# Optimization experiments

Measured on AMD Instinct MI355X. Metric: run time of the kernel, lower is better.

The kernel has to match this reference:

```python
import jax, jax.numpy as jnp
import numpy as np

N_NODES = 100000
N_EDGES = 640000
IN_DIM = 64
HIDDEN = 128
N_STEPS = 5
NUM_CLASSES = 2


def _gru_cell(a, h, w_ih, w_hh, b_ih, b_hh):
    # PyTorch GRUCell: gates ordered (reset, update, new)
    gi = a @ w_ih.T + b_ih   # [N, 3H]
    gh = h @ w_hh.T + b_hh   # [N, 3H]
    i_r, i_z, i_n = jnp.split(gi, 3, axis=-1)
    h_r, h_z, h_n = jnp.split(gh, 3, axis=-1)
    r = jax.nn.sigmoid(i_r + h_r)
    z = jax.nn.sigmoid(i_z + h_z)
    n = jnp.tanh(i_n + r * h_n)
    return (1.0 - z) * n + z * h


def _gated_graph_conv(feat, src, dst, W, b, w_ih, w_hh, b_ih, b_hh):
    # DGL GatedGraphConv with a single edge type:
    #   pad input to out_feats, then n_steps of
    #   a = sum_{incoming edges} Linear(h[src]); h = GRUCell(a, h)
    n = feat.shape[0]
    pad = HIDDEN - feat.shape[1]
    h = jnp.pad(feat, ((0, 0), (0, pad))) if pad > 0 else feat
    for _ in range(N_STEPS):
        m = h @ W.T + b                                  # [N, H] edge-type linear
        a = jax.ops.segment_sum(m[src], dst, num_segments=n)  # gather + scatter-sum
        h = _gru_cell(a, h, w_ih, w_hh, b_ih, b_hh)
    return h


def setup_inputs() -> dict:
    key = jax.random.key(0)
    ks = jax.random.split(key, 16)
    s = 0.05
    inp = {
        "features": jax.random.normal(ks[0], (N_NODES, IN_DIM), dtype=jnp.float32),
        "src": jax.random.randint(ks[1], (N_EDGES,), 0, N_NODES, dtype=jnp.int32),
        "dst": jax.random.randint(ks[2], (N_EDGES,), 0, N_NODES, dtype=jnp.int32),
        # layer 1 (in 64 -> padded to 128)
        "W1": jax.random.normal(ks[3], (HIDDEN, HIDDEN), dtype=jnp.float32) * s,
        "b1": jnp.zeros((HIDDEN,), dtype=jnp.float32),
        "gru1_w_ih": jax.random.normal(ks[4], (3 * HIDDEN, HIDDEN), dtype=jnp.float32) * s,
        "gru1_w_hh": jax.random.normal(ks[5], (3 * HIDDEN, HIDDEN), dtype=jnp.float32) * s,
        "gru1_b_ih": jnp.zeros((3 * HIDDEN,), dtype=jnp.float32),
        "gru1_b_hh": jnp.zeros((3 * HIDDEN,), dtype=jnp.float32),
        # layer 2 (128 -> 128)
        "W2": jax.random.normal(ks[6], (HIDDEN, HIDDEN), dtype=jnp.float32) * s,
        "b2": jnp.zeros((HIDDEN,), dtype=jnp.float32),
        "gru2_w_ih": jax.random.normal(ks[7], (3 * HIDDEN, HIDDEN), dtype=jnp.float32) * s,
        "gru2_w_hh": jax.random.normal(ks[8], (3 * HIDDEN, HIDDEN), dtype=jnp.float32) * s,
        "gru2_b_ih": jnp.zeros((3 * HIDDEN,), dtype=jnp.float32),
        "gru2_b_hh": jnp.zeros((3 * HIDDEN,), dtype=jnp.float32),
        # classifier head
        "fc_w": jax.random.normal(ks[9], (NUM_CLASSES, HIDDEN), dtype=jnp.float32) * s,
        "fc_b": jnp.zeros((NUM_CLASSES,), dtype=jnp.float32),
    }
    return inp


def reference(features, src, dst,
              W1, b1, gru1_w_ih, gru1_w_hh, gru1_b_ih, gru1_b_hh,
              W2, b2, gru2_w_ih, gru2_w_hh, gru2_b_ih, gru2_b_hh,
              fc_w, fc_b):
    h = _gated_graph_conv(features, src, dst, W1, b1, gru1_w_ih, gru1_w_hh, gru1_b_ih, gru1_b_hh)
    h = _gated_graph_conv(h, src, dst, W2, b2, gru2_w_ih, gru2_w_hh, gru2_b_ih, gru2_b_hh)
    return h @ fc_w.T + fc_b  # [N, num_classes]
```

## Files before the change

### kernel.cpp

```cpp
#include <hip/hip_runtime.h>

#define N_HID 128
typedef unsigned short u16;
typedef unsigned int u32;
typedef __attribute__((ext_vector_type(8))) short bfrag;
typedef __attribute__((ext_vector_type(4))) float facc;

__device__ __forceinline__ float sigf(float x) { return 1.f / (1.f + __expf(-x)); }
__device__ __forceinline__ float tanh_fast(float x) { return 1.f - 2.f / (__expf(2.f * x) + 1.f); }
__device__ __forceinline__ u16 f2bf(float f) {
  u32 u = __float_as_uint(f);
  u += 0x7fffu + ((u >> 16) & 1u);
  return (u16)(u >> 16);
}
__device__ __forceinline__ float bf2f(u16 b) { return __uint_as_float(((u32)b) << 16); }

__global__ __launch_bounds__(256) void wihw_kernel(const float* __restrict__ wih,
                                                   const float* __restrict__ W,
                                                   float* __restrict__ out) {
  int i = blockIdx.x * 256 + threadIdx.x;
  if (i >= 49152) return;
  int gc = i >> 7, k = i & 127;
  float acc = 0.f;
  for (int c = 0; c < 128; c++) acc = fmaf(wih[gc * 128 + c], W[c * 128 + k], acc);
  out[i] = acc;
}

__global__ __launch_bounds__(256) void wb_kernel(const float* __restrict__ wih,
                                                 const float* __restrict__ b,
                                                 float* __restrict__ wb) {
  int gc = blockIdx.x * 256 + threadIdx.x;
  if (gc >= 384) return;
  float acc = 0.f;
  for (int c = 0; c < 128; c++) acc = fmaf(wih[gc * 128 + c], b[c], acc);
  wb[gc] = acc;
}

__global__ __launch_bounds__(128) void pack_bias_kernel(const float* __restrict__ bih,
                                                        const float* __restrict__ bhh,
                                                        const float* __restrict__ wb,
                                                        float* __restrict__ PB7) {
  int ch = threadIdx.x;
  PB7[ch * 8 + 0] = bih[ch] + bhh[ch];
  PB7[ch * 8 + 1] = bih[128 + ch] + bhh[128 + ch];
  PB7[ch * 8 + 2] = bih[256 + ch];
  PB7[ch * 8 + 3] = bhh[256 + ch];
  PB7[ch * 8 + 4] = wb[ch];
  PB7[ch * 8 + 5] = wb[128 + ch];
  PB7[ch * 8 + 6] = wb[256 + ch];
  PB7[ch * 8 + 7] = 0.f;
}

__global__ __launch_bounds__(256) void pack_gru_kernel(const float* __restrict__ wih,
                                                       const float* __restrict__ whh,
                                                       u16* __restrict__ GB) {
  int i = blockIdx.x * 256 + threadIdx.x;
  if (i >= 131072) return;
  int e = i & 7, l = (i >> 3) & 63, pct = (i >> 9) & 31, kt = i >> 14;
  int cw = pct >> 3, t = pct & 7, kind = t >> 1, sub = t & 1;
  int ch = cw * 32 + ((l & 15) << 1) + sub;
  int k = kt * 32 + ((l >> 4) << 3) + e;
  float v = 0.f;
  if (kind == 0) v = (k < 128) ? wih[ch * 128 + k] : whh[ch * 128 + k - 128];
  else if (kind == 1) v = (k < 128) ? wih[(128 + ch) * 128 + k] : whh[(128 + ch) * 128 + k - 128];
  else if (kind == 2) v = (k < 128) ? wih[(256 + ch) * 128 + k] : 0.f;
  else v = (k >= 128) ? whh[(256 + ch) * 128 + k - 128] : 0.f;
  GB[i] = f2bf(v);
}

__global__ __launch_bounds__(256) void pad_bf_kernel(const float* __restrict__ feat,
                                                     u16* __restrict__ hbf, int n) {
  int i = blockIdx.x * 256 + threadIdx.x;
  if (i >= n * 32) return;
  int node = i >> 5, c4 = i & 31;
  float4 v = make_float4(0.f, 0.f, 0.f, 0.f);
  if (c4 < 16) v = ((const float4*)feat)[(size_t)node * 16 + c4];
  u32 p0 = (u32)f2bf(v.x) | ((u32)f2bf(v.y) << 16);
  u32 p1 = (u32)f2bf(v.z) | ((u32)f2bf(v.w) << 16);
  ((uint2*)hbf)[i] = make_uint2(p0, p1);
}

__global__ __launch_bounds__(256) void hist_kernel(const int* __restrict__ dst,
                                                   int* __restrict__ deg, int E) {
  int e = blockIdx.x * 256 + threadIdx.x;
  if (e < E) atomicAdd(&deg[dst[e]], 1);
}

__global__ __launch_bounds__(256) void scan1_kernel(const int* __restrict__ deg,
                                                    int* __restrict__ out,
                                                    int* __restrict__ bsums, int n) {
  __shared__ int s[256];
  int t = threadIdx.x;
  int base = blockIdx.x * 4096 + t * 16;
  int v[16];
  int local = 0;
#pragma unroll
  for (int i = 0; i < 16; i++) {
    int x = (base + i < n) ? deg[base + i] : 0;
    v[i] = local;
    local += x;
  }
  s[t] = local;
  __syncthreads();
  for (int off = 1; off < 256; off <<= 1) {
    int add = (t >= off) ? s[t - off] : 0;
    __syncthreads();
    s[t] += add;
    __syncthreads();
  }
  int texcl = s[t] - local;
#pragma unroll
  for (int i = 0; i < 16; i++)
    if (base + i < n) out[base + i] = texcl + v[i];
  if (t == 255) bsums[blockIdx.x] = s[255];
}

__global__ __launch_bounds__(256) void scan_tops_kernel(int* __restrict__ bsums, int nb) {
  __shared__ int s[256];
  int t = threadIdx.x;
  int orig = (t < nb) ? bsums[t] : 0;
  s[t] = orig;
  __syncthreads();
  for (int off = 1; off < 256; off <<= 1) {
    int add = (t >= off) ? s[t - off] : 0;
    __syncthreads();
    s[t] += add;
    __syncthreads();
  }
  if (t < nb) bsums[t] = s[t] - orig;
}

__global__ __launch_bounds__(256) void scan_add_kernel(int* __restrict__ rowptr,
                                                       const int* __restrict__ bsums,
                                                       int n, int E) {
  int i = blockIdx.x * 256 + threadIdx.x;
  if (i < n) rowptr[i] += bsums[i / 4096];
  if (i == n) rowptr[n] = E;
}

__global__ __launch_bounds__(256) void bucket_kernel(const int* __restrict__ src,
                                                     const int* __restrict__ dst,
                                                     const int* __restrict__ rowptr,
                                                     int* __restrict__ cursor,
                                                     int* __restrict__ csr_src, int E) {
  int e = blockIdx.x * 256 + threadIdx.x;
  if (e >= E) return;
  int d = dst[e];
  int p = atomicAdd(&cursor[d], 1);
  csr_src[rowptr[d] + p] = src[e] * 16;
}

__global__ __launch_bounds__(512) void gru_fused_kernel(const u16* __restrict__ hbf_in,
                                                        u16* __restrict__ hbf_out,
                                                        const u16* __restrict__ GB,
                                                        const float* __restrict__ PB7,
                                                        const int* __restrict__ rowptr,
                                                        const int* __restrict__ csr_src,
                                                        const int* __restrict__ deg, int n) {
  __shared__ __align__(16) u16 sX[64 * 256];
  __shared__ float sD[64];
  const int tid = threadIdx.x;
  const int base = blockIdx.x * 64;

  if (tid < 64) {
    int gn = base + tid;
    if (gn >= n) gn = n - 1;
    sD[tid] = (float)deg[gn];
  }
  for (int it = 0; it < 2; it++) {
    int cid = it * 512 + tid;
    int node = cid >> 4, cc = cid & 15;
    int gn = base + node;
    if (gn >= n) gn = n - 1;
    uint4 v = ((const uint4*)hbf_in)[(size_t)gn * 16 + cc];
    int c = 16 + cc;
    *(uint4*)((char*)sX + node * 512 + ((c ^ (node & 7)) << 4)) = v;
  }

  {
    int node = tid >> 3, p = tid & 7;
    int gn = base + node;
    if (gn >= n) gn = n - 1;
    int beg = rowptr[gn], end = rowptr[gn + 1];
    float acc[16];
#pragma unroll
    for (int i = 0; i < 16; i++) acc[i] = 0.f;
#define ACC8(v, o)                                                       \
    acc[o + 0] += bf2f((u16)((v).x & 0xffff)); acc[o + 1] += bf2f((u16)((v).x >> 16)); \
    acc[o + 2] += bf2f((u16)((v).y & 0xffff)); acc[o + 3] += bf2f((u16)((v).y >> 16)); \
    acc[o + 4] += bf2f((u16)((v).z & 0xffff)); acc[o + 5] += bf2f((u16)((v).z >> 16)); \
    acc[o + 6] += bf2f((u16)((v).w & 0xffff)); acc[o + 7] += bf2f((u16)((v).w >> 16));
    const uint4* hp = (const uint4*)hbf_in + 2 * p;
    int j = beg;
    int nA = (j < end) ? csr_src[j] : 0;
    int nB = (j + 1 < end) ? csr_src[j + 1] : 0;
    for (; j + 1 < end; j += 2) {
      int o0 = nA, o1 = nB;
      nA = (j + 2 < end) ? csr_src[j + 2] : 0;
      nB = (j + 3 < end) ? csr_src[j + 3] : 0;
      uint4 a0 = hp[o0];
      uint4 a1 = hp[o0 + 1];
      uint4 b0 = hp[o1];
      uint4 b1 = hp[o1 + 1];
      ACC8(a0, 0); ACC8(a1, 8); ACC8(b0, 0); ACC8(b1, 8);
    }
    if (j < end) {
      int o0 = nA;
      uint4 a0 = hp[o0];
      uint4 a1 = hp[o0 + 1];
      ACC8(a0, 0); ACC8(a1, 8);
    }
#undef ACC8
    uint4 w0, w1;
    w0.x = (u32)f2bf(acc[0])  | ((u32)f2bf(acc[1])  << 16);
    w0.y = (u32)f2bf(acc[2])  | ((u32)f2bf(acc[3])  << 16);
    w0.z = (u32)f2bf(acc[4])  | ((u32)f2bf(acc[5])  << 16);
    w0.w = (u32)f2bf(acc[6])  | ((u32)f2bf(acc[7])  << 16);
    w1.x = (u32)f2bf(acc[8])  | ((u32)f2bf(acc[9])  << 16);
    w1.y = (u32)f2bf(acc[10]) | ((u32)f2bf(acc[11]) << 16);
    w1.z = (u32)f2bf(acc[12]) | ((u32)f2bf(acc[13]) << 16);
    w1.w = (u32)f2bf(acc[14]) | ((u32)f2bf(acc[15]) << 16);
    *(uint4*)((char*)sX + node * 512 + (((2 * p)     ^ (node & 7)) << 4)) = w0;
    *(uint4*)((char*)sX + node * 512 + (((2 * p + 1) ^ (node & 7)) << 4)) = w1;
  }
  __syncthreads();

  const int w = tid >> 6, l = tid & 63;
  const int cw = w & 3, nh = w >> 2;
  facc accR[2][2], accZ[2][2], accIN[2][2], accHN[2][2];
#pragma unroll
  for (int i = 0; i < 2; i++)
#pragma unroll
    for (int j = 0; j < 2; j++) {
      accR[i][j] = (facc)(0.f); accZ[i][j] = (facc)(0.f);
      accIN[i][j] = (facc)(0.f); accHN[i][j] = (facc)(0.f);
    }

#pragma unroll
  for (int kt = 0; kt < 8; kt++) {
    bfrag A[2];
#pragma unroll
    for (int rt = 0; rt < 2; rt++) {
      int row = nh * 32 + rt * 16 + (l & 15);
      int slot = kt * 4 + (l >> 4);
      A[rt] = *(const bfrag*)((const char*)sX + row * 512 + ((slot ^ (row & 7)) << 4));
    }
    const bfrag* gb = (const bfrag*)GB + (size_t)(kt * 32 + cw * 8) * 64 + l;
#pragma unroll
    for (int s2 = 0; s2 < 2; s2++) {
      bfrag Br = gb[s2 * 64];
      bfrag Bz = gb[(2 + s2) * 64];
#pragma unroll
      for (int rt = 0; rt < 2; rt++) {
        accR[rt][s2] = __builtin_amdgcn_mfma_f32_16x16x32_bf16(A[rt], Br, accR[rt][s2], 0, 0, 0);
        accZ[rt][s2] = __builtin_amdgcn_mfma_f32_16x16x32_bf16(A[rt], Bz, accZ[rt][s2], 0, 0, 0);
      }
    }
    if (kt < 4) {
#pragma unroll
      for (int s2 = 0; s2 < 2; s2++) {
        bfrag Bi = gb[(4 + s2) * 64];
#pragma unroll
        for (int rt = 0; rt < 2; rt++)
          accIN[rt][s2] = __builtin_amdgcn_mfma_f32_16x16x32_bf16(A[rt], Bi, accIN[rt][s2], 0, 0, 0);
      }
    } else {
#pragma unroll
      for (int s2 = 0; s2 < 2; s2++) {
        bfrag Bh = gb[(6 + s2) * 64];
#pragma unroll
        for (int rt = 0; rt < 2; rt++)
          accHN[rt][s2] = __builtin_amdgcn_mfma_f32_16x16x32_bf16(A[rt], Bh, accHN[rt][s2], 0, 0, 0);
      }
    }
  }

  {
    int m = l & 15;
    int ch0 = cw * 32 + (m << 1);
    const float4* pb = (const float4*)(PB7 + ch0 * 8);
    float4 c0a = pb[0], c0b = pb[1];
    float4 c1a = pb[2], c1b = pb[3];
    int hc = 16 + (ch0 >> 3);
    int hb = (ch0 & 7) * 2;
#pragma unroll
    for (int rt = 0; rt < 2; rt++)
#pragma unroll
      for (int j = 0; j < 4; j++) {
        int gl = nh * 32 + rt * 16 + ((l >> 4) << 2) + j;
        int g = base + gl;
        float dg = sD[gl];
        u32 hop = *(const u32*)((const char*)sX + gl * 512 + ((hc ^ (gl & 7)) << 4) + hb);
        float ho0 = bf2f((u16)(hop & 0xffff));
        float ho1 = bf2f((u16)(hop >> 16));
        float r0 = sigf(accR[rt][0][j] + dg * c0b.x + c0a.x);
        float z0 = sigf(accZ[rt][0][j] + dg * c0b.y + c0a.y);
        float nn0 = tanh_fast(accIN[rt][0][j] + dg * c0b.z + c0a.z + r0 * (accHN[rt][0][j] + c0a.w));
        float hn0 = (1.f - z0) * nn0 + z0 * ho0;
        float r1 = sigf(accR[rt][1][j] + dg * c1b.x + c1a.x);
        float z1 = sigf(accZ[rt][1][j] + dg * c1b.y + c1a.y);
        float nn1 = tanh_fast(accIN[rt][1][j] + dg * c1b.z + c1a.z + r1 * (accHN[rt][1][j] + c1a.w));
        float hn1 = (1.f - z1) * nn1 + z1 * ho1;
        if (g < n)
          *(u32*)&hbf_out[(size_t)g * 128 + ch0] = (u32)f2bf(hn0) | ((u32)f2bf(hn1) << 16);
      }
  }
}

__global__ __launch_bounds__(256) void head_kernel(const u16* __restrict__ hbf,
                                                   const float* __restrict__ fc_w,
                                                   const float* __restrict__ fc_b,
                                                   float* __restrict__ out, int n) {
  int wave = (blockIdx.x * 256 + threadIdx.x) >> 6;
  int lane = threadIdx.x & 63;
  if (wave >= n) return;
  u32 hv = ((const u32*)hbf)[(size_t)wave * 64 + lane];
  float h0 = bf2f((u16)(hv & 0xffff)), h1 = bf2f((u16)(hv >> 16));
  float2 w0 = ((const float2*)fc_w)[lane];
  float2 w1 = ((const float2*)fc_w)[64 + lane];
  float p0 = h0 * w0.x + h1 * w0.y;
  float p1 = h0 * w1.x + h1 * w1.y;
#pragma unroll
  for (int off = 32; off > 0; off >>= 1) {
    p0 += __shfl_down(p0, off, 64);
    p1 += __shfl_down(p1, off, 64);
  }
  if (lane == 0) {
    out[(size_t)wave * 2 + 0] = p0 + fc_b[0];
    out[(size_t)wave * 2 + 1] = p1 + fc_b[1];
  }
}

extern "C" void kernel_launch(void* const* d_in, const int* in_sizes, int n_in,
                              void* d_out, int out_size, void* d_ws, size_t ws_size,
                              hipStream_t stream) {
  const float* feat = (const float*)d_in[0];
  const int* src = (const int*)d_in[1];
  const int* dst = (const int*)d_in[2];
  const int N = in_sizes[0] / 64;
  const int E = in_sizes[1];

  const float* Wl[2]  = {(const float*)d_in[3], (const float*)d_in[9]};
  const float* bl[2]  = {(const float*)d_in[4], (const float*)d_in[10]};
  const float* wih[2] = {(const float*)d_in[5], (const float*)d_in[11]};
  const float* whh[2] = {(const float*)d_in[6], (const float*)d_in[12]};
  const float* bih[2] = {(const float*)d_in[7], (const float*)d_in[13]};
  const float* bhh[2] = {(const float*)d_in[8], (const float*)d_in[14]};
  const float* fcw = (const float*)d_in[15];
  const float* fcb = (const float*)d_in[16];

  u16* hbf0 = (u16*)d_ws;
  u16* hbf1 = hbf0 + (size_t)N * 128;
  float* WIH2[2];
  WIH2[0] = (float*)(hbf1 + (size_t)N * 128);
  WIH2[1] = WIH2[0] + 49152;
  float* wb2[2] = {WIH2[1] + 49152, WIH2[1] + 49152 + 384};
  u16* GB[2];
  GB[0] = (u16*)(wb2[1] + 384);
  GB[1] = GB[0] + 131072;
  float* PB7[2];
  PB7[0] = (float*)(GB[1] + 131072);
  PB7[1] = PB7[0] + 1024;
  int* rowptr = (int*)(PB7[1] + 1024);
  int* deg = rowptr + (N + 1);
  int* csr_src = deg + N;
  int* bsums = csr_src + E;

  for (int l = 0; l < 2; l++) {
    wihw_kernel<<<192, 256, 0, stream>>>(wih[l], Wl[l], WIH2[l]);
    wb_kernel<<<2, 256, 0, stream>>>(wih[l], bl[l], wb2[l]);
    pack_gru_kernel<<<512, 256, 0, stream>>>(WIH2[l], whh[l], GB[l]);
    pack_bias_kernel<<<1, 128, 0, stream>>>(bih[l], bhh[l], wb2[l], PB7[l]);
  }
  pad_bf_kernel<<<(N * 32 + 255) / 256, 256, 0, stream>>>(feat, hbf0, N);

  int nb = (N + 4095) / 4096;
  hipMemsetAsync(deg, 0, (size_t)N * sizeof(int), stream);
  hist_kernel<<<(E + 255) / 256, 256, 0, stream>>>(dst, deg, E);
  scan1_kernel<<<nb, 256, 0, stream>>>(deg, rowptr, bsums, N);
  scan_tops_kernel<<<1, 256, 0, stream>>>(bsums, nb);
  scan_add_kernel<<<(N + 256) / 256, 256, 0, stream>>>(rowptr, bsums, N, E);
  hipMemsetAsync(deg, 0, (size_t)N * sizeof(int), stream);
  bucket_kernel<<<(E + 255) / 256, 256, 0, stream>>>(src, dst, rowptr, deg, csr_src, E);

  u16* hb[2] = {hbf0, hbf1};
  int cur = 0;
  int nblk = (N + 63) / 64;
  for (int layer = 0; layer < 2; layer++) {
    for (int step = 0; step < 5; step++) {
      gru_fused_kernel<<<nblk, 512, 0, stream>>>(hb[cur], hb[cur ^ 1], GB[layer], PB7[layer],
                                                 rowptr, csr_src, deg, N);
      cur ^= 1;
    }
  }

  head_kernel<<<(N + 3) / 4, 256, 0, stream>>>(hb[cur], fcw, fcb, (float*)d_out, N);
}
```

Measured before the change: 877.8 us.

## Sort nodes by in-degree and process GRU blocks in degree order

Adds a counting sort of nodes by in-degree (histogram, scan, atomic scatter into a permutation). The fused gather+GRU kernel then processes nodes through this permutation, so each 64-node block holds nodes of similar degree. The goal is less warp and block load imbalance in the neighbour-gather loop. In exchange, row reads and writes of a node's own state are no longer contiguous across a block, and a few small preprocessing kernels are added.

```diff
diff --git a/kernel.cpp b/kernel.cpp
--- a/kernel.cpp
+++ b/kernel.cpp
@@ -150,38 +150,58 @@
   csr_src[rowptr[d] + p] = src[e] * 16;
 }
 
+__global__ __launch_bounds__(256) void deg_hist_kernel(const int* __restrict__ deg,
+                                                       int* __restrict__ dhist, int n) {
+  int i = blockIdx.x * 256 + threadIdx.x;
+  if (i < n) atomicAdd(&dhist[min(deg[i], 255)], 1);
+}
+
+__global__ __launch_bounds__(256) void perm_scatter_kernel(const int* __restrict__ deg,
+                                                           int* __restrict__ dbase,
+                                                           int* __restrict__ perm, int n) {
+  int i = blockIdx.x * 256 + threadIdx.x;
+  if (i >= n) return;
+  int d = min(deg[i], 255);
+  int pos = atomicAdd(&dbase[d], 1);
+  perm[pos] = i;
+}
+
 __global__ __launch_bounds__(512) void gru_fused_kernel(const u16* __restrict__ hbf_in,
                                                         u16* __restrict__ hbf_out,
                                                         const u16* __restrict__ GB,
                                                         const float* __restrict__ PB7,
                                                         const int* __restrict__ rowptr,
                                                         const int* __restrict__ csr_src,
-                                                        const int* __restrict__ deg, int n) {
+                                                        const int* __restrict__ deg,
+                                                        const int* __restrict__ perm, int n) {
   __shared__ __align__(16) u16 sX[64 * 256];
   __shared__ float sD[64];
+  __shared__ int sP[64];
   const int tid = threadIdx.x;
   const int base = blockIdx.x * 64;
 
   if (tid < 64) {
-    int gn = base + tid;
-    if (gn >= n) gn = n - 1;
-    sD[tid] = (float)deg[gn];
-  }
+    int pidx = base + tid;
+    if (pidx >= n) pidx = n - 1;
+    int pn = perm[pidx];
+    sP[tid] = pn;
+    sD[tid] = (float)deg[pn];
+  }
+  __syncthreads();
+
   for (int it = 0; it < 2; it++) {
     int cid = it * 512 + tid;
     int node = cid >> 4, cc = cid & 15;
-    int gn = base + node;
-    if (gn >= n) gn = n - 1;
-    uint4 v = ((const uint4*)hbf_in)[(size_t)gn * 16 + cc];
+    int pn = sP[node];
+    uint4 v = ((const uint4*)hbf_in)[(size_t)pn * 16 + cc];
     int c = 16 + cc;
     *(uint4*)((char*)sX + node * 512 + ((c ^ (node & 7)) << 4)) = v;
   }
 
   {
     int node = tid >> 3, p = tid & 7;
-    int gn = base + node;
-    if (gn >= n) gn = n - 1;
-    int beg = rowptr[gn], end = rowptr[gn + 1];
+    int pn = sP[node];
+    int beg = rowptr[pn], end = rowptr[pn + 1];
     float acc[16];
 #pragma unroll
     for (int i = 0; i < 16; i++) acc[i] = 0.f;
@@ -288,7 +308,6 @@
 #pragma unroll
       for (int j = 0; j < 4; j++) {
         int gl = nh * 32 + rt * 16 + ((l >> 4) << 2) + j;
-        int g = base + gl;
         float dg = sD[gl];
         u32 hop = *(const u32*)((const char*)sX + gl * 512 + ((hc ^ (gl & 7)) << 4) + hb);
         float ho0 = bf2f((u16)(hop & 0xffff));
@@ -301,8 +320,7 @@
         float z1 = sigf(accZ[rt][1][j] + dg * c1b.y + c1a.y);
         float nn1 = tanh_fast(accIN[rt][1][j] + dg * c1b.z + c1a.z + r1 * (accHN[rt][1][j] + c1a.w));
         float hn1 = (1.f - z1) * nn1 + z1 * ho1;
-        if (g < n)
-          *(u32*)&hbf_out[(size_t)g * 128 + ch0] = (u32)f2bf(hn0) | ((u32)f2bf(hn1) << 16);
+        *(u32*)&hbf_out[(size_t)sP[gl] * 128 + ch0] = (u32)f2bf(hn0) | ((u32)f2bf(hn1) << 16);
       }
   }
 }
@@ -365,6 +383,8 @@
   int* deg = rowptr + (N + 1);
   int* csr_src = deg + N;
   int* bsums = csr_src + E;
+  int* dhist = bsums + 256;
+  int* perm = dhist + 256;
 
   for (int l = 0; l < 2; l++) {
     wihw_kernel<<<192, 256, 0, stream>>>(wih[l], Wl[l], WIH2[l]);
@@ -383,13 +403,18 @@
   hipMemsetAsync(deg, 0, (size_t)N * sizeof(int), stream);
   bucket_kernel<<<(E + 255) / 256, 256, 0, stream>>>(src, dst, rowptr, deg, csr_src, E);
 
+  hipMemsetAsync(dhist, 0, 256 * sizeof(int), stream);
+  deg_hist_kernel<<<(N + 255) / 256, 256, 0, stream>>>(deg, dhist, N);
+  scan_tops_kernel<<<1, 256, 0, stream>>>(dhist, 256);
+  perm_scatter_kernel<<<(N + 255) / 256, 256, 0, stream>>>(deg, dhist, perm, N);
+
   u16* hb[2] = {hbf0, hbf1};
   int cur = 0;
   int nblk = (N + 63) / 64;
   for (int layer = 0; layer < 2; layer++) {
     for (int step = 0; step < 5; step++) {
       gru_fused_kernel<<<nblk, 512, 0, stream>>>(hb[cur], hb[cur ^ 1], GB[layer], PB7[layer],
-                                                 rowptr, csr_src, deg, N);
+                                                 rowptr, csr_src, deg, perm, N);
       cur ^= 1;
     }
   }
```

Result: slower. 1.793 ms (+104.2%).
